# Optimization experiments

Measured on AMD Instinct MI355X. Metric: run time of the kernel, lower is better.

Reference implementation:

```python
import jax, jax.numpy as jnp
import numpy as np

B, N, K = 4, 4096, 16
D_PTS, D_MODEL = 64, 128


def setup_inputs() -> dict:
    key = jax.random.key(0)
    ks = jax.random.split(key, 18)
    w = lambda k_, shape, fan: (jax.random.normal(k_, shape, jnp.float32) / np.sqrt(fan))
    return {
        "xyz": jax.random.normal(ks[0], (B, N, 3), jnp.float32),
        "features": jax.random.normal(ks[1], (B, N, D_PTS), jnp.float32),
        "w_fc1": w(ks[2], (D_PTS, D_MODEL), D_PTS),
        "b_fc1": jnp.zeros((D_MODEL,), jnp.float32),
        "w_fc2": w(ks[3], (D_MODEL, D_PTS), D_MODEL),
        "b_fc2": jnp.zeros((D_PTS,), jnp.float32),
        "w_d1": w(ks[4], (3, D_MODEL), 3),
        "b_d1": jnp.zeros((D_MODEL,), jnp.float32),
        "w_d2": w(ks[5], (D_MODEL, D_MODEL), D_MODEL),
        "b_d2": jnp.zeros((D_MODEL,), jnp.float32),
        "w_g1": w(ks[6], (D_MODEL, D_MODEL), D_MODEL),
        "b_g1": jnp.zeros((D_MODEL,), jnp.float32),
        "w_g2": w(ks[7], (D_MODEL, D_MODEL), D_MODEL),
        "b_g2": jnp.zeros((D_MODEL,), jnp.float32),
        "w_q": w(ks[8], (D_MODEL, D_MODEL), D_MODEL),
        "w_k": w(ks[9], (D_MODEL, D_MODEL), D_MODEL),
        "w_v": w(ks[10], (D_MODEL, D_MODEL), D_MODEL),
    }


def reference(xyz, features, w_fc1, b_fc1, w_fc2, b_fc2,
              w_d1, b_d1, w_d2, b_d2, w_g1, b_g1, w_g2, b_g2,
              w_q, w_k, w_v):
    # --- kNN: squared pairwise distances, take K smallest ---
    sq = jnp.sum(xyz * xyz, axis=-1)                       # (B, N)
    d2 = sq[:, :, None] + sq[:, None, :] - 2.0 * jnp.einsum('bnd,bmd->bnm', xyz, xyz)
    _, knn_idx = jax.lax.top_k(-d2, K)                     # (B, N, K) int32
    bidx = jnp.arange(B)[:, None, None]

    knn_xyz = xyz[bidx, knn_idx]                           # (B, N, K, 3)
    pre = features
    x = features @ w_fc1 + b_fc1                           # (B, N, D_MODEL)

    q = x @ w_q                                            # (B, N, D_MODEL)
    k_g = (x @ w_k)[bidx, knn_idx]                         # (B, N, K, D_MODEL)
    v_g = (x @ w_v)[bidx, knn_idx]                         # (B, N, K, D_MODEL)

    rel = xyz[:, :, None] - knn_xyz                        # (B, N, K, 3)
    pos_enc = jax.nn.relu(rel @ w_d1 + b_d1) @ w_d2 + b_d2 # (B, N, K, D_MODEL)

    attn = jax.nn.relu((q[:, :, None] - k_g + pos_enc) @ w_g1 + b_g1) @ w_g2 + b_g2
    attn = jax.nn.softmax(attn / np.sqrt(D_MODEL).astype(np.float32), axis=-2)

    res = jnp.einsum('bmnf,bmnf->bmf', attn, v_g + pos_enc)  # (B, N, D_MODEL)
    res = res @ w_fc2 + b_fc2 + pre                          # (B, N, D_PTS)
    return res, attn
```

## Files before the change

### kernel.cpp

```cpp
#include <hip/hip_runtime.h>
#include <math.h>

#define BATCH 4
#define NPTS 4096
#define KNN 16
#define DPTS 64
#define DM 128

typedef __attribute__((ext_vector_type(8))) short short8;
typedef __attribute__((ext_vector_type(4))) float floatx4;
typedef __attribute__((ext_vector_type(4))) unsigned int uintx4;

static __device__ __forceinline__ float bf2f(unsigned short h) {
    union { unsigned int u; float f; } c; c.u = ((unsigned int)h) << 16; return c.f;
}
static __device__ __forceinline__ unsigned short f2bf(float f) {
    union { float f; unsigned int u; } c; c.f = f;
    unsigned int u = c.u;
    u += 0x7fffu + ((u >> 16) & 1u);
    return (unsigned short)(u >> 16);
}

__global__ __launch_bounds__(256) void knn_kernel(const float* __restrict__ xyz,
                                                  int* __restrict__ knn_idx) {
    extern __shared__ char smem[];
    float* sxx = (float*)smem;
    float* sxy = sxx + 4100;
    float* sxz = sxy + 4100;
    float* md  = sxz + 4100;
    unsigned short* mi = (unsigned short*)(md + 4096);

    int b = blockIdx.x >> 6;
    int qbase = (blockIdx.x & 63) * 64;
    const float* bx = xyz + b * NPTS * 3;
    for (int j = threadIdx.x; j < NPTS; j += 256) {
        int jj = j + (j >> 10);
        sxx[jj] = bx[j*3+0];
        sxy[jj] = bx[j*3+1];
        sxz[jj] = bx[j*3+2];
    }
    __syncthreads();

    int q = qbase + (threadIdx.x >> 2);
    int s = threadIdx.x & 3;
    int qjj = q + (q >> 10);
    float qx = sxx[qjj], qy = sxy[qjj], qz = sxz[qjj];
    float qsq = __fadd_rn(__fadd_rn(__fmul_rn(qx, qx), __fmul_rn(qy, qy)), __fmul_rn(qz, qz));

    float bd0=3.0e38f,bd1=3.0e38f,bd2=3.0e38f,bd3=3.0e38f,bd4=3.0e38f,bd5=3.0e38f,bd6=3.0e38f,bd7=3.0e38f,
          bd8=3.0e38f,bd9=3.0e38f,bd10=3.0e38f,bd11=3.0e38f,bd12=3.0e38f,bd13=3.0e38f,bd14=3.0e38f,bd15=3.0e38f;
    int bi0=0,bi1=0,bi2=0,bi3=0,bi4=0,bi5=0,bi6=0,bi7=0,
        bi8=0,bi9=0,bi10=0,bi11=0,bi12=0,bi13=0,bi14=0,bi15=0;

#define INS1(t) { bool sm = cur_d < bd##t; float td = bd##t; int ti = bi##t; \
                  bd##t = sm ? cur_d : td; bi##t = sm ? cur_i : ti;          \
                  cur_d = sm ? td : cur_d; cur_i = sm ? ti : cur_i; }

    int j0 = s << 10;
    int jj0 = s * 1025;
    for (int m = 0; m < 1024; ++m) {
        float xj = sxx[jj0 + m], yj = sxy[jj0 + m], zj = sxz[jj0 + m];
        float sqj = __fadd_rn(__fadd_rn(__fmul_rn(xj, xj), __fmul_rn(yj, yj)), __fmul_rn(zj, zj));
        float dot = __fadd_rn(__fadd_rn(__fmul_rn(qx, xj), __fmul_rn(qy, yj)), __fmul_rn(qz, zj));
        float d = __fsub_rn(__fadd_rn(qsq, sqj), __fmul_rn(2.0f, dot));
        if (d < bd15) {
            float cur_d = d; int cur_i = j0 + m;
            INS1(0) INS1(1) INS1(2) INS1(3) INS1(4) INS1(5) INS1(6) INS1(7)
            INS1(8) INS1(9) INS1(10) INS1(11) INS1(12) INS1(13) INS1(14) INS1(15)
        }
    }
#undef INS1

    {
        int base = threadIdx.x * 16;
        md[base+0]=bd0;  mi[base+0]=(unsigned short)bi0;
        md[base+1]=bd1;  mi[base+1]=(unsigned short)bi1;
        md[base+2]=bd2;  mi[base+2]=(unsigned short)bi2;
        md[base+3]=bd3;  mi[base+3]=(unsigned short)bi3;
        md[base+4]=bd4;  mi[base+4]=(unsigned short)bi4;
        md[base+5]=bd5;  mi[base+5]=(unsigned short)bi5;
        md[base+6]=bd6;  mi[base+6]=(unsigned short)bi6;
        md[base+7]=bd7;  mi[base+7]=(unsigned short)bi7;
        md[base+8]=bd8;  mi[base+8]=(unsigned short)bi8;
        md[base+9]=bd9;  mi[base+9]=(unsigned short)bi9;
        md[base+10]=bd10; mi[base+10]=(unsigned short)bi10;
        md[base+11]=bd11; mi[base+11]=(unsigned short)bi11;
        md[base+12]=bd12; mi[base+12]=(unsigned short)bi12;
        md[base+13]=bd13; mi[base+13]=(unsigned short)bi13;
        md[base+14]=bd14; mi[base+14]=(unsigned short)bi14;
        md[base+15]=bd15; mi[base+15]=(unsigned short)bi15;
    }
    __syncthreads();
    if (s == 0) {
        int r = threadIdx.x * 16;
        int p0=0,p1=0,p2=0,p3=0;
        int out_base = (b*NPTS + q) * KNN;
        #pragma unroll
        for (int t = 0; t < 16; ++t) {
            float d0 = md[r+p0];    int i0 = mi[r+p0];
            float d1 = md[r+16+p1]; int i1 = mi[r+16+p1];
            float d2 = md[r+32+p2]; int i2 = mi[r+32+p2];
            float d3 = md[r+48+p3]; int i3 = mi[r+48+p3];
            float bdv = d0; int bii = i0; int which = 0;
            if (d1 < bdv || (d1 == bdv && i1 < bii)) { bdv=d1; bii=i1; which=1; }
            if (d2 < bdv || (d2 == bdv && i2 < bii)) { bdv=d2; bii=i2; which=2; }
            if (d3 < bdv || (d3 == bdv && i3 < bii)) { bdv=d3; bii=i3; which=3; }
            knn_idx[out_base + t] = bii;
            if (which==0) p0++; else if (which==1) p1++; else if (which==2) p2++; else p3++;
        }
    }
}

__global__ __launch_bounds__(256) void pack_kernel(const float* __restrict__ w_d2,
                                                   const float* __restrict__ w_g1,
                                                   const float* __restrict__ w_g2,
                                                   unsigned short* __restrict__ wpack) {
    int t = blockIdx.x * 256 + threadIdx.x;
    if (t >= 3*4*8*64) return;
    int lane = t & 63;
    int nt = (t >> 6) & 7;
    int kt = (t >> 9) & 3;
    int g  = t >> 11;
    const float* w = (g == 0) ? w_d2 : (g == 1) ? w_g1 : w_g2;
    int colbase = nt*16 + (lane & 15);
    int kbase   = kt*32 + (lane >> 4)*8;
    union { unsigned short us[8]; uintx4 v; } u;
    #pragma unroll
    for (int i = 0; i < 8; ++i) u.us[i] = f2bf(w[(kbase+i)*DM + colbase]);
    ((uintx4*)wpack)[t] = u.v;
}

__global__ __launch_bounds__(256) void qkv_kernel(
    const float* __restrict__ features, const float* __restrict__ w_fc1, const float* __restrict__ b_fc1,
    const float* __restrict__ w_q, const float* __restrict__ w_k, const float* __restrict__ w_v,
    unsigned short* __restrict__ qo, unsigned short* __restrict__ ko, unsigned short* __restrict__ vo) {
    extern __shared__ char smem[];
    float* sfeat = (float*)smem;
    float* sxbuf = (float*)(smem + 16384);
    float* swt   = (float*)(smem + 16384 + 32768);
    int rowbase = blockIdx.x * 64;

    for (int t = threadIdx.x; t < 64*64/4; t += 256)
        ((float4*)sfeat)[t] = ((const float4*)(features + rowbase*DPTS))[t];
    for (int t = threadIdx.x; t < 64*DM/4; t += 256)
        ((float4*)swt)[t] = ((const float4*)w_fc1)[t];
    __syncthreads();

    int r  = threadIdx.x >> 2;
    int cg = (threadIdx.x & 3) * 32;
    {
        float acc[32];
        #pragma unroll
        for (int cc = 0; cc < 32; ++cc) acc[cc] = b_fc1[cg + cc];
        for (int h = 0; h < 64; ++h) {
            float f = sfeat[r*64 + h];
            #pragma unroll
            for (int cc = 0; cc < 32; ++cc) acc[cc] += f * swt[h*DM + cg + cc];
        }
        #pragma unroll
        for (int cc = 0; cc < 32; ++cc) sxbuf[r*DM + cg + cc] = acc[cc];
    }
    __syncthreads();

    for (int g = 0; g < 3; ++g) {
        const float* wsrc = (g == 0) ? w_q : (g == 1) ? w_k : w_v;
        unsigned short* op = ((g == 0) ? qo : (g == 1) ? ko : vo) + (rowbase + r)*DM + cg;
        for (int t = threadIdx.x; t < DM*DM/4; t += 256)
            ((float4*)swt)[t] = ((const float4*)wsrc)[t];
        __syncthreads();
        float a2[32];
        #pragma unroll
        for (int cc = 0; cc < 32; ++cc) a2[cc] = 0.f;
        for (int h = 0; h < DM; ++h) {
            float xv = sxbuf[r*DM + h];
            #pragma unroll
            for (int cc = 0; cc < 32; ++cc) a2[cc] += xv * swt[h*DM + cg + cc];
        }
        #pragma unroll
        for (int cc = 0; cc < 32; ++cc) op[cc] = f2bf(a2[cc]);
        __syncthreads();
    }
}

__global__ __launch_bounds__(256) void main_kernel(
    const float* __restrict__ xyz, const float* __restrict__ features,
    const float* __restrict__ w_fc2, const float* __restrict__ b_fc2,
    const float* __restrict__ w_d1, const float* __restrict__ b_d1,
    const float* __restrict__ b_d2, const float* __restrict__ b_g1, const float* __restrict__ b_g2,
    const unsigned short* __restrict__ qg, const unsigned short* __restrict__ kg,
    const unsigned short* __restrict__ vg,
    const int* __restrict__ knn_idx, const unsigned short* __restrict__ wpack,
    float* __restrict__ res_out, float* __restrict__ attn_out) {
    extern __shared__ char smem[];
    unsigned short* swp = (unsigned short*)smem;
    float* sw_d1 = (float*)(smem + 98304);
    float* sb_d1 = (float*)(smem + 99840);
    float* sb_d2 = (float*)(smem + 100352);
    float* sb_g1 = (float*)(smem + 100864);
    float* sb_g2 = (float*)(smem + 101376);

    for (int t = threadIdx.x; t < 98304/16; t += 256)
        ((uintx4*)swp)[t] = ((const uintx4*)wpack)[t];
    for (int t = threadIdx.x; t < 384; t += 256) sw_d1[t] = w_d1[t];
    if (threadIdx.x < 128) {
        sb_d1[threadIdx.x] = b_d1[threadIdx.x];
        sb_d2[threadIdx.x] = b_d2[threadIdx.x];
        sb_g1[threadIdx.x] = b_g1[threadIdx.x];
        sb_g2[threadIdx.x] = b_g2[threadIdx.x];
    }
    __syncthreads();

    int wave = threadIdx.x >> 6;
    int lane = threadIdx.x & 63;
    int nbr  = lane & 15;
    int cblk = lane >> 4;
    char* wbase = smem + 101888 + wave * 13056;
    unsigned short* pe_l = (unsigned short*)wbase;
    unsigned short* a1_l = (unsigned short*)(wbase + 4096);
    unsigned short* v_l  = (unsigned short*)(wbase + 8192);
    float* rel_l = (float*)(wbase + 12288);
    int*   idx_l = (int*)(wbase + 12480);
    float* res_l = (float*)(wbase + 12544);

    const float inv_sqrt_d = 0.08838834764831845f;

    for (int pt = 0; pt < 4; ++pt) {
        int p = (blockIdx.x * 4 + wave) * 4 + pt;
        int b = p >> 12, n = p & 4095;
        int pbase = b * NPTS + n;

        if (lane < 16) {
            int id = knn_idx[pbase*KNN + lane];
            idx_l[lane] = id;
            const float* cp = xyz + (b*NPTS + id)*3;
            const float* qp = xyz + pbase*3;
            rel_l[lane*3+0] = qp[0] - cp[0];
            rel_l[lane*3+1] = qp[1] - cp[1];
            rel_l[lane*3+2] = qp[2] - cp[2];
        }
        __syncthreads();

        int myidx = idx_l[nbr];
        {
            const unsigned short* vp = vg + (b*NPTS + myidx)*DM;
            #pragma unroll
            for (int kt = 0; kt < 4; ++kt) {
                int c8 = kt*32 + cblk*8;
                uintx4 vr = *((const uintx4*)(vp + c8));
                int byte = (nbr*256 + c8*2) ^ ((nbr & 7) << 4);
                *(uintx4*)(( char*)v_l + byte) = vr;
            }
        }
        short8 af[4];
        {
            float r0 = rel_l[nbr*3+0], r1 = rel_l[nbr*3+1], r2 = rel_l[nbr*3+2];
            #pragma unroll
            for (int kt = 0; kt < 4; ++kt) {
                #pragma unroll
                for (int i = 0; i < 8; ++i) {
                    int c = kt*32 + cblk*8 + i;
                    float h = r0*sw_d1[c] + r1*sw_d1[DM + c] + r2*sw_d1[2*DM + c] + sb_d1[c];
                    h = fmaxf(h, 0.f);
                    af[kt][i] = (short)f2bf(h);
                }
            }
        }
        for (int nt = 0; nt < 8; ++nt) {
            floatx4 acc = {0.f, 0.f, 0.f, 0.f};
            #pragma unroll
            for (int kt = 0; kt < 4; ++kt) {
                short8 bf = *((const short8*)(swp + ((0*4 + kt)*8 + nt)*512 + lane*8));
                acc = __builtin_amdgcn_mfma_f32_16x16x32_bf16(af[kt], bf, acc, 0, 0, 0);
            }
            int c = nt*16 + nbr;
            #pragma unroll
            for (int rg = 0; rg < 4; ++rg) {
                int krow = cblk*4 + rg;
                float pv = acc[rg] + sb_d2[c];
                int byte = (krow*256 + c*2) ^ ((krow & 7) << 4);
                *(unsigned short*)((char*)pe_l + byte) = f2bf(pv);
            }
        }
        __syncthreads();

        short8 tf[4];
        {
            const unsigned short* kp = kg + (b*NPTS + myidx)*DM;
            const unsigned short* qp = qg + pbase*DM;
            #pragma unroll
            for (int kt = 0; kt < 4; ++kt) {
                int c8 = kt*32 + cblk*8;
                uintx4 kr = *((const uintx4*)(kp + c8));
                uintx4 qr = *((const uintx4*)(qp + c8));
                int byte = (nbr*256 + c8*2) ^ ((nbr & 7) << 4);
                uintx4 pr = *(const uintx4*)((char*)pe_l + byte);
                #pragma unroll
                for (int w2 = 0; w2 < 4; ++w2) {
                    float k0 = bf2f((unsigned short)(kr[w2] & 0xffffu));
                    float k1 = bf2f((unsigned short)(kr[w2] >> 16));
                    float q0 = bf2f((unsigned short)(qr[w2] & 0xffffu));
                    float q1 = bf2f((unsigned short)(qr[w2] >> 16));
                    float p0 = bf2f((unsigned short)(pr[w2] & 0xffffu));
                    float p1 = bf2f((unsigned short)(pr[w2] >> 16));
                    tf[kt][w2*2]   = (short)f2bf(q0 - k0 + p0);
                    tf[kt][w2*2+1] = (short)f2bf(q1 - k1 + p1);
                }
            }
        }
        for (int nt = 0; nt < 8; ++nt) {
            floatx4 acc = {0.f, 0.f, 0.f, 0.f};
            #pragma unroll
            for (int kt = 0; kt < 4; ++kt) {
                short8 bf = *((const short8*)(swp + ((1*4 + kt)*8 + nt)*512 + lane*8));
                acc = __builtin_amdgcn_mfma_f32_16x16x32_bf16(tf[kt], bf, acc, 0, 0, 0);
            }
            int c = nt*16 + nbr;
            #pragma unroll
            for (int rg = 0; rg < 4; ++rg) {
                int krow = cblk*4 + rg;
                float av = fmaxf(acc[rg] + sb_g1[c], 0.f);
                int byte = (krow*256 + c*2) ^ ((krow & 7) << 4);
                *(unsigned short*)((char*)a1_l + byte) = f2bf(av);
            }
        }
        __syncthreads();

        short8 a1f[4];
        #pragma unroll
        for (int kt = 0; kt < 4; ++kt) {
            int c8 = kt*32 + cblk*8;
            int byte = (nbr*256 + c8*2) ^ ((nbr & 7) << 4);
            a1f[kt] = *(const short8*)((char*)a1_l + byte);
        }
        for (int nt = 0; nt < 8; ++nt) {
            floatx4 acc = {0.f, 0.f, 0.f, 0.f};
            #pragma unroll
            for (int kt = 0; kt < 4; ++kt) {
                short8 bf = *((const short8*)(swp + ((2*4 + kt)*8 + nt)*512 + lane*8));
                acc = __builtin_amdgcn_mfma_f32_16x16x32_bf16(a1f[kt], bf, acc, 0, 0, 0);
            }
            int c = nt*16 + nbr;
            float s[4];
            #pragma unroll
            for (int rg = 0; rg < 4; ++rg) s[rg] = (acc[rg] + sb_g2[c]) * inv_sqrt_d;
            float mx = fmaxf(fmaxf(s[0], s[1]), fmaxf(s[2], s[3]));
            mx = fmaxf(mx, __shfl_xor(mx, 16));
            mx = fmaxf(mx, __shfl_xor(mx, 32));
            float e[4]; float sum = 0.f;
            #pragma unroll
            for (int rg = 0; rg < 4; ++rg) { e[rg] = __expf(s[rg] - mx); sum += e[rg]; }
            sum += __shfl_xor(sum, 16);
            sum += __shfl_xor(sum, 32);
            float inv = 1.f / sum;
            float rpart = 0.f;
            #pragma unroll
            for (int rg = 0; rg < 4; ++rg) {
                float a = e[rg] * inv;
                int krow = cblk*4 + rg;
                attn_out[(pbase*KNN + krow)*DM + c] = a;
                int byte = (krow*256 + c*2) ^ ((krow & 7) << 4);
                float vv = bf2f(*(const unsigned short*)((char*)v_l + byte));
                float pv = bf2f(*(const unsigned short*)((char*)pe_l + byte));
                rpart += a * (vv + pv);
            }
            rpart += __shfl_xor(rpart, 16);
            rpart += __shfl_xor(rpart, 32);
            if (lane < 16) res_l[nt*16 + lane] = rpart;
        }
        __syncthreads();

        {
            float accr = 0.f;
            #pragma unroll 4
            for (int c = 0; c < DM; ++c) accr += res_l[c] * w_fc2[c*DPTS + lane];
            res_out[pbase*DPTS + lane] = accr + b_fc2[lane] + features[pbase*DPTS + lane];
        }
        __syncthreads();
    }
}

extern "C" void kernel_launch(void* const* d_in, const int* in_sizes, int n_in,
                              void* d_out, int out_size, void* d_ws, size_t ws_size,
                              hipStream_t stream) {
    const float* xyz      = (const float*)d_in[0];
    const float* features = (const float*)d_in[1];
    const float* w_fc1    = (const float*)d_in[2];
    const float* b_fc1    = (const float*)d_in[3];
    const float* w_fc2    = (const float*)d_in[4];
    const float* b_fc2    = (const float*)d_in[5];
    const float* w_d1     = (const float*)d_in[6];
    const float* b_d1     = (const float*)d_in[7];
    const float* w_d2     = (const float*)d_in[8];
    const float* b_d2     = (const float*)d_in[9];
    const float* w_g1     = (const float*)d_in[10];
    const float* b_g1     = (const float*)d_in[11];
    const float* w_g2     = (const float*)d_in[12];
    const float* b_g2     = (const float*)d_in[13];
    const float* w_q      = (const float*)d_in[14];
    const float* w_k      = (const float*)d_in[15];
    const float* w_v      = (const float*)d_in[16];

    char* ws = (char*)d_ws;
    int* knn            = (int*)ws;
    unsigned short* qb  = (unsigned short*)(ws + (1 << 20));
    unsigned short* kb  = (unsigned short*)(ws + (5 << 20));
    unsigned short* vb  = (unsigned short*)(ws + (9 << 20));
    unsigned short* wpk = (unsigned short*)(ws + (13 << 20));

    float* res_out  = (float*)d_out;
    float* attn_out = res_out + BATCH*NPTS*DPTS;

    pack_kernel<<<dim3(24), dim3(256), 0, stream>>>(w_d2, w_g1, w_g2, wpk);
    knn_kernel<<<dim3(256), dim3(256), 73776, stream>>>(xyz, knn);
    qkv_kernel<<<dim3(256), dim3(256), 114688, stream>>>(features, w_fc1, b_fc1,
                                                         w_q, w_k, w_v, qb, kb, vb);
    main_kernel<<<dim3(1024), dim3(256), 154112, stream>>>(
        xyz, features, w_fc2, b_fc2, w_d1, b_d1, b_d2, b_g1, b_g2,
        qb, kb, vb, knn, wpk, res_out, attn_out);
}
```

Measured before the change: 904.0 us.

## Split kNN scan 8 ways, precompute norms, use wave-local fences in main kernel

The kNN kernel now uses 8 threads per query over 512-point slices with 32 queries per block and twice as many blocks. Per-point squared norms are precomputed once into shared memory, and the merge step is widened to an 8-way merge that reuses the coordinate buffer. In the main kernel, block-wide barriers between per-wave stages are replaced by an LDS waitcnt plus scheduling barrier, on the premise that each wave only touches its own LDS region. This aims to raise parallelism in the kNN scan and cut barrier stalls, at the cost of a longer merge and reliance on wave-private shared data.

```diff
diff --git a/kernel.cpp b/kernel.cpp
--- a/kernel.cpp
+++ b/kernel.cpp
@@ -11,6 +11,9 @@
 typedef __attribute__((ext_vector_type(4))) float floatx4;
 typedef __attribute__((ext_vector_type(4))) unsigned int uintx4;
 
+#define WFENCE() do { asm volatile("s_waitcnt lgkmcnt(0)" ::: "memory"); \
+                      __builtin_amdgcn_sched_barrier(0); } while (0)
+
 static __device__ __forceinline__ float bf2f(unsigned short h) {
     union { unsigned int u; float f; } c; c.u = ((unsigned int)h) << 16; return c.f;
 }
@@ -25,27 +28,28 @@
                                                   int* __restrict__ knn_idx) {
     extern __shared__ char smem[];
     float* sxx = (float*)smem;
-    float* sxy = sxx + 4100;
-    float* sxz = sxy + 4100;
-    float* md  = sxz + 4100;
-    unsigned short* mi = (unsigned short*)(md + 4096);
-
-    int b = blockIdx.x >> 6;
-    int qbase = (blockIdx.x & 63) * 64;
+    float* sxy = sxx + 4104;
+    float* sxz = sxy + 4104;
+    float* ssq = sxz + 4104;
+    float* md          = (float*)smem;
+    unsigned short* mi = (unsigned short*)(smem + 16384);
+
+    int b = blockIdx.x >> 7;
+    int qbase = (blockIdx.x & 127) * 32;
     const float* bx = xyz + b * NPTS * 3;
     for (int j = threadIdx.x; j < NPTS; j += 256) {
-        int jj = j + (j >> 10);
-        sxx[jj] = bx[j*3+0];
-        sxy[jj] = bx[j*3+1];
-        sxz[jj] = bx[j*3+2];
-    }
-    __syncthreads();
-
-    int q = qbase + (threadIdx.x >> 2);
-    int s = threadIdx.x & 3;
-    int qjj = q + (q >> 10);
+        int jj = j + (j >> 9);
+        float x = bx[j*3+0], y = bx[j*3+1], z = bx[j*3+2];
+        sxx[jj] = x; sxy[jj] = y; sxz[jj] = z;
+        ssq[jj] = __fadd_rn(__fadd_rn(__fmul_rn(x, x), __fmul_rn(y, y)), __fmul_rn(z, z));
+    }
+    __syncthreads();
+
+    int q = qbase + (threadIdx.x >> 3);
+    int s = threadIdx.x & 7;
+    int qjj = q + (q >> 9);
     float qx = sxx[qjj], qy = sxy[qjj], qz = sxz[qjj];
-    float qsq = __fadd_rn(__fadd_rn(__fmul_rn(qx, qx), __fmul_rn(qy, qy)), __fmul_rn(qz, qz));
+    float qsq = ssq[qjj];
 
     float bd0=3.0e38f,bd1=3.0e38f,bd2=3.0e38f,bd3=3.0e38f,bd4=3.0e38f,bd5=3.0e38f,bd6=3.0e38f,bd7=3.0e38f,
           bd8=3.0e38f,bd9=3.0e38f,bd10=3.0e38f,bd11=3.0e38f,bd12=3.0e38f,bd13=3.0e38f,bd14=3.0e38f,bd15=3.0e38f;
@@ -56,11 +60,11 @@
                   bd##t = sm ? cur_d : td; bi##t = sm ? cur_i : ti;          \
                   cur_d = sm ? td : cur_d; cur_i = sm ? ti : cur_i; }
 
-    int j0 = s << 10;
-    int jj0 = s * 1025;
-    for (int m = 0; m < 1024; ++m) {
+    int j0 = s << 9;
+    int jj0 = 513 * s;
+    for (int m = 0; m < 512; ++m) {
         float xj = sxx[jj0 + m], yj = sxy[jj0 + m], zj = sxz[jj0 + m];
-        float sqj = __fadd_rn(__fadd_rn(__fmul_rn(xj, xj), __fmul_rn(yj, yj)), __fmul_rn(zj, zj));
+        float sqj = ssq[jj0 + m];
         float dot = __fadd_rn(__fadd_rn(__fmul_rn(qx, xj), __fmul_rn(qy, yj)), __fmul_rn(qz, zj));
         float d = __fsub_rn(__fadd_rn(qsq, sqj), __fmul_rn(2.0f, dot));
         if (d < bd15) {
@@ -71,6 +75,7 @@
     }
 #undef INS1
 
+    __syncthreads();
     {
         int base = threadIdx.x * 16;
         md[base+0]=bd0;  mi[base+0]=(unsigned short)bi0;
@@ -93,20 +98,21 @@
     __syncthreads();
     if (s == 0) {
         int r = threadIdx.x * 16;
-        int p0=0,p1=0,p2=0,p3=0;
+        int p0=0,p1=0,p2=0,p3=0,p4=0,p5=0,p6=0,p7=0;
         int out_base = (b*NPTS + q) * KNN;
         #pragma unroll
         for (int t = 0; t < 16; ++t) {
-            float d0 = md[r+p0];    int i0 = mi[r+p0];
-            float d1 = md[r+16+p1]; int i1 = mi[r+16+p1];
-            float d2 = md[r+32+p2]; int i2 = mi[r+32+p2];
-            float d3 = md[r+48+p3]; int i3 = mi[r+48+p3];
-            float bdv = d0; int bii = i0; int which = 0;
-            if (d1 < bdv || (d1 == bdv && i1 < bii)) { bdv=d1; bii=i1; which=1; }
-            if (d2 < bdv || (d2 == bdv && i2 < bii)) { bdv=d2; bii=i2; which=2; }
-            if (d3 < bdv || (d3 == bdv && i3 < bii)) { bdv=d3; bii=i3; which=3; }
+            float bdv = md[r+p0];      int bii = mi[r+p0];      int which = 0;
+            { float dd = md[r+16+p1];  int ii = mi[r+16+p1];  if (dd < bdv || (dd == bdv && ii < bii)) { bdv=dd; bii=ii; which=1; } }
+            { float dd = md[r+32+p2];  int ii = mi[r+32+p2];  if (dd < bdv || (dd == bdv && ii < bii)) { bdv=dd; bii=ii; which=2; } }
+            { float dd = md[r+48+p3];  int ii = mi[r+48+p3];  if (dd < bdv || (dd == bdv && ii < bii)) { bdv=dd; bii=ii; which=3; } }
+            { float dd = md[r+64+p4];  int ii = mi[r+64+p4];  if (dd < bdv || (dd == bdv && ii < bii)) { bdv=dd; bii=ii; which=4; } }
+            { float dd = md[r+80+p5];  int ii = mi[r+80+p5];  if (dd < bdv || (dd == bdv && ii < bii)) { bdv=dd; bii=ii; which=5; } }
+            { float dd = md[r+96+p6];  int ii = mi[r+96+p6];  if (dd < bdv || (dd == bdv && ii < bii)) { bdv=dd; bii=ii; which=6; } }
+            { float dd = md[r+112+p7]; int ii = mi[r+112+p7]; if (dd < bdv || (dd == bdv && ii < bii)) { bdv=dd; bii=ii; which=7; } }
             knn_idx[out_base + t] = bii;
-            if (which==0) p0++; else if (which==1) p1++; else if (which==2) p2++; else p3++;
+            if (which==0) p0++; else if (which==1) p1++; else if (which==2) p2++; else if (which==3) p3++;
+            else if (which==4) p4++; else if (which==5) p5++; else if (which==6) p6++; else p7++;
         }
     }
 }
@@ -238,7 +244,7 @@
             rel_l[lane*3+1] = qp[1] - cp[1];
             rel_l[lane*3+2] = qp[2] - cp[2];
         }
-        __syncthreads();
+        WFENCE();
 
         int myidx = idx_l[nbr];
         {
@@ -281,7 +287,7 @@
                 *(unsigned short*)((char*)pe_l + byte) = f2bf(pv);
             }
         }
-        __syncthreads();
+        WFENCE();
 
         short8 tf[4];
         {
@@ -323,7 +329,7 @@
                 *(unsigned short*)((char*)a1_l + byte) = f2bf(av);
             }
         }
-        __syncthreads();
+        WFENCE();
 
         short8 a1f[4];
         #pragma unroll
@@ -367,7 +373,7 @@
             rpart += __shfl_xor(rpart, 32);
             if (lane < 16) res_l[nt*16 + lane] = rpart;
         }
-        __syncthreads();
+        WFENCE();
 
         {
             float accr = 0.f;
@@ -375,7 +381,7 @@
             for (int c = 0; c < DM; ++c) accr += res_l[c] * w_fc2[c*DPTS + lane];
             res_out[pbase*DPTS + lane] = accr + b_fc2[lane] + features[pbase*DPTS + lane];
         }
-        __syncthreads();
+        WFENCE();
     }
 }
 
@@ -411,7 +417,7 @@
     float* attn_out = res_out + BATCH*NPTS*DPTS;
 
     pack_kernel<<<dim3(24), dim3(256), 0, stream>>>(w_d2, w_g1, w_g2, wpk);
-    knn_kernel<<<dim3(256), dim3(256), 73776, stream>>>(xyz, knn);
+    knn_kernel<<<dim3(512), dim3(256), 65664, stream>>>(xyz, knn);
     qkv_kernel<<<dim3(256), dim3(256), 114688, stream>>>(features, w_fc1, b_fc1,
                                                          w_q, w_k, w_v, qb, kb, vb);
     main_kernel<<<dim3(1024), dim3(256), 154112, stream>>>(
```

New measurement: 858.1 us. 1.05x faster.
